# Optimization experiments

Measured on AMD Instinct MI355X. Metric: run time of the kernel, lower is better.

Reference implementation:

```python
import jax, jax.numpy as jnp
import numpy as np

S, B, D, H, O = 128, 16, 512, 512, 256  # seq_len, batch, input=hidden (required equal), hidden, output

def setup_inputs() -> dict:
    key = jax.random.key(0)
    ks = jax.random.split(key, 11)
    sD = 1.0 / np.sqrt(D)
    sH = 1.0 / np.sqrt(H)
    g = lambda k, shape, s: (jax.random.normal(k, shape, dtype=jnp.float32) * s)
    return {
        "x": g(ks[0], (S, B, D), 1.0),
        # LocalAttention (undefined in source; feature-wise softmax gating): Linear(H,H)
        "attn_w": g(ks[1], (D, H), sD), "attn_b": g(ks[2], (H,), sD),
        "in_w": g(ks[3], (D, H), sD), "in_b": g(ks[4], (H,), sD),      # the_in
        "ins_w": g(ks[5], (H, H), sH), "ins_b": g(ks[6], (H,), sH),    # inside
        "sus_w": g(ks[7], (H, H), sH), "sus_b": g(ks[8], (H,), sH),    # suspend_state
        "out_w": g(ks[9], (H, O), sH), "out_b": g(ks[10], (O,), sH),   # output_layer
    }

def reference(x, attn_w, attn_b, in_w, in_b, ins_w, ins_b, sus_w, sus_b, out_w, out_b):
    S_, B_, _ = x.shape
    H_ = ins_w.shape[0]

    def step(carry, read):
        watch, sus = carry  # both [S,B,H] per the original broadcasting bug/behavior
        a = jax.nn.softmax(read @ attn_w + attn_b, axis=-1)  # [B,H]
        r = a * read                                          # [B,D]
        # [B,H] broadcasts over leading S dim of [S,B,H]
        watch = jnp.tanh((r @ in_w + in_b) + (watch @ ins_w + ins_b))
        sus = jnp.tanh((watch @ sus_w + sus_b) + sus)
        out = watch @ out_w + out_b                           # [S,B,O]
        return (watch, sus), out

    init = (jnp.zeros((S_, B_, H_), x.dtype), jnp.zeros((S_, B_, H_), x.dtype))
    (watch, sus), outs = jax.lax.scan(step, init, x)  # outs: [S,S,B,O]
    return outs, watch, sus
```

## Files before the change

### kernel.cpp

```cpp
#include <hip/hip_runtime.h>
#include <hip/hip_bf16.h>
#include <math.h>


#define S_LEN 128
#define B_SZ  16
#define H_SZ  512
#define O_SZ  256
#define ROWS  (S_LEN * B_SZ)

#define OUTS_ELEMS  (S_LEN * S_LEN * B_SZ * O_SZ)
#define WATCH_ELEMS (S_LEN * B_SZ * H_SZ)

typedef float  f32x4  __attribute__((ext_vector_type(4)));
typedef __bf16 bf16x8 __attribute__((ext_vector_type(8)));

struct alignas(16) GemmLds {
  __bf16 Ah[64][40]; __bf16 Al[64][40];
  __bf16 Bh[64][40]; __bf16 Bl[64][40];
};

__device__ __forceinline__ void gemm_body(
    const float* __restrict__ A, const float* __restrict__ B,
    const float* __restrict__ bias0, const float* __restrict__ bias1,
    float* __restrict__ C, int N, int K, int bm, int bn, GemmLds& T)
{
  const int tid = threadIdx.x;
  const int w = tid >> 6, l = tid & 63;
  const int fr = l & 15, fg = l >> 4;
  f32x4 acc[4] = {{0,0,0,0},{0,0,0,0},{0,0,0,0},{0,0,0,0}};
  const int ar = tid >> 2, ak = (tid & 3) << 3;
  const int bk = tid >> 3, bc = (tid & 7) << 3;

  for (int k0 = 0; k0 < K; k0 += 32) {
    {
      const float* s = &A[(size_t)(bm + ar) * K + k0 + ak];
      const f32x4 v0 = *(const f32x4*)s, v1 = *(const f32x4*)(s + 4);
      const float vv[8] = {v0.x, v0.y, v0.z, v0.w, v1.x, v1.y, v1.z, v1.w};
      bf16x8 h, lo;
#pragma unroll
      for (int j = 0; j < 8; ++j) {
        const __bf16 hh = (__bf16)vv[j];
        h[j] = hh; lo[j] = (__bf16)(vv[j] - (float)hh);
      }
      *(bf16x8*)&T.Ah[ar][ak] = h;
      *(bf16x8*)&T.Al[ar][ak] = lo;
    }
    {
      const float* s = &B[(size_t)(k0 + bk) * N + bn + bc];
      const f32x4 v0 = *(const f32x4*)s, v1 = *(const f32x4*)(s + 4);
      const float vv[8] = {v0.x, v0.y, v0.z, v0.w, v1.x, v1.y, v1.z, v1.w};
#pragma unroll
      for (int j = 0; j < 8; ++j) {
        const __bf16 hh = (__bf16)vv[j];
        T.Bh[bc + j][bk] = hh;
        T.Bl[bc + j][bk] = (__bf16)(vv[j] - (float)hh);
      }
    }
    __syncthreads();
    const bf16x8 ah = *(const bf16x8*)&T.Ah[(w << 4) + fr][fg << 3];
    const bf16x8 al = *(const bf16x8*)&T.Al[(w << 4) + fr][fg << 3];
#pragma unroll
    for (int nr = 0; nr < 4; ++nr) {
      const bf16x8 bh = *(const bf16x8*)&T.Bh[(nr << 4) + fr][fg << 3];
      const bf16x8 bl = *(const bf16x8*)&T.Bl[(nr << 4) + fr][fg << 3];
      acc[nr] = __builtin_amdgcn_mfma_f32_16x16x32_bf16(ah, bh, acc[nr], 0, 0, 0);
      acc[nr] = __builtin_amdgcn_mfma_f32_16x16x32_bf16(al, bh, acc[nr], 0, 0, 0);
      acc[nr] = __builtin_amdgcn_mfma_f32_16x16x32_bf16(ah, bl, acc[nr], 0, 0, 0);
    }
    __syncthreads();
  }
#pragma unroll
  for (int nr = 0; nr < 4; ++nr) {
    const int gcol = bn + (nr << 4) + fr;
    float bb = bias0 ? bias0[gcol] : 0.f;
    if (bias1) bb += bias1[gcol];
#pragma unroll
    for (int r = 0; r < 4; ++r) {
      const int grow = bm + (w << 4) + (fg << 2) + r;
      C[(size_t)grow * N + gcol] = acc[nr][r] + bb;
    }
  }
}

__global__ __launch_bounds__(256) void gemm_mfma(
    const float* __restrict__ A, const float* __restrict__ B,
    const float* __restrict__ bias0, const float* __restrict__ bias1,
    float* __restrict__ C, int N, int K)
{
  __shared__ GemmLds T;
  gemm_body(A, B, bias0, bias1, C, N, K, blockIdx.y << 6, blockIdx.x << 6, T);
}

__global__ __launch_bounds__(256) void gemm_dual_mfma(
    const float* __restrict__ A,
    const float* __restrict__ B1, const float* __restrict__ b1, float* __restrict__ C1,
    const float* __restrict__ B2, const float* __restrict__ b2, float* __restrict__ C2)
{
  __shared__ GemmLds T;
  if (blockIdx.x < 8)
    gemm_body(A, B1, b1, nullptr, C1, 512, 512, blockIdx.y << 6, blockIdx.x << 6, T);
  else
    gemm_body(A, B2, b2, nullptr, C2, 256, 512, blockIdx.y << 6, (blockIdx.x - 8) << 6, T);
}

__global__ __launch_bounds__(64) void softmax_gate(float* __restrict__ lg,
                                                   const float* __restrict__ x)
{
  const int r = blockIdx.x;
  const int lane = threadIdx.x;
  float v[8];
  float m = -1e30f;
#pragma unroll
  for (int i = 0; i < 8; ++i) {
    v[i] = lg[(r << 9) + (i << 6) + lane];
    m = fmaxf(m, v[i]);
  }
#pragma unroll
  for (int off = 32; off > 0; off >>= 1) m = fmaxf(m, __shfl_xor(m, off, 64));
  float s = 0.f;
#pragma unroll
  for (int i = 0; i < 8; ++i) { v[i] = expf(v[i] - m); s += v[i]; }
#pragma unroll
  for (int off = 32; off > 0; off >>= 1) s += __shfl_xor(s, off, 64);
  const float inv = 1.0f / s;
#pragma unroll
  for (int i = 0; i < 8; ++i) {
    const int idx = (r << 9) + (i << 6) + lane;
    lg[idx] = v[i] * inv * x[idx];
  }
}

__global__ __launch_bounds__(256, 1) void recurrence(
    const float* __restrict__ cbuf,
    const float* __restrict__ insw,
    float* __restrict__ wall,
    unsigned long long* __restrict__ pz)
{
  __shared__ float wsm[H_SZ];
  __shared__ float red[2][4][64];

  const int wg  = blockIdx.x;
  const int b   = wg & 15;
  const int p   = wg >> 4;
  const int tid = threadIdx.x;
  const int cl  = tid & 63;
  const int kq  = tid >> 6;
  const int c   = (p << 6) + cl;
  const int kbase = kq << 7;

  f32x4 wr[32];
#pragma unroll
  for (int j = 0; j < 32; ++j) {
    wr[j].x = insw[((kbase + 4 * j + 0) << 9) + c];
    wr[j].y = insw[((kbase + 4 * j + 1) << 9) + c];
    wr[j].z = insw[((kbase + 4 * j + 2) << 9) + c];
    wr[j].w = insw[((kbase + 4 * j + 3) << 9) + c];
  }

  if (tid < 64) {
    const float v = tanhf(cbuf[(b << 9) + c]);
    wall[(b << 9) + c] = v;
    const unsigned long long pk =
        (1ULL << 32) | (unsigned long long)__float_as_uint(v);
    __hip_atomic_store(&pz[(b << 9) + c], pk, __ATOMIC_RELAXED,
                       __HIP_MEMORY_SCOPE_AGENT);
  }

  for (int t = 1; t < S_LEN; ++t) {
    const float cv = cbuf[(t << 13) + (b << 9) + c];

    const unsigned long long* src =
        pz + (((t - 1) & 15) << 13) + (b << 9);
    unsigned long long v0, v1;
    for (;;) {
      v0 = __hip_atomic_load(&src[2 * tid], __ATOMIC_RELAXED,
                             __HIP_MEMORY_SCOPE_AGENT);
      v1 = __hip_atomic_load(&src[2 * tid + 1], __ATOMIC_RELAXED,
                             __HIP_MEMORY_SCOPE_AGENT);
      const bool ok = ((unsigned)(v0 >> 32) == (unsigned)t) &
                      ((unsigned)(v1 >> 32) == (unsigned)t);
      if (__ballot(ok) == ~0ULL) break;
    }
    wsm[2 * tid]     = __uint_as_float((unsigned)v0);
    wsm[2 * tid + 1] = __uint_as_float((unsigned)v1);
    asm volatile("s_waitcnt lgkmcnt(0)" ::: "memory");
    __builtin_amdgcn_sched_barrier(0);

    float a0 = 0.f, a1 = 0.f, a2 = 0.f, a3 = 0.f;
#pragma unroll
    for (int j = 0; j < 32; ++j) {
      const f32x4 wv = *(const f32x4*)&wsm[kbase + (j << 2)];
      a0 = fmaf(wr[j].x, wv.x, a0);
      a1 = fmaf(wr[j].y, wv.y, a1);
      a2 = fmaf(wr[j].z, wv.z, a2);
      a3 = fmaf(wr[j].w, wv.w, a3);
    }
    red[t & 1][kq][cl] = (a0 + a1) + (a2 + a3);
    __syncthreads();
    if (tid < 64) {
      const float y = red[t & 1][0][cl] + red[t & 1][1][cl] +
                      red[t & 1][2][cl] + red[t & 1][3][cl];
      const float v = tanhf(cv + y);
      wall[(t << 13) + (b << 9) + c] = v;
      const unsigned long long pk =
          ((unsigned long long)(unsigned)(t + 1) << 32) |
          (unsigned long long)__float_as_uint(v);
      __hip_atomic_store(&pz[((t & 15) << 13) + (b << 9) + c], pk,
                         __ATOMIC_RELAXED, __HIP_MEMORY_SCOPE_AGENT);
    }
  }
}

__global__ __launch_bounds__(256) void sus_scan(
    const float* __restrict__ M, float* __restrict__ s_small)
{
  const int gid = blockIdx.x * blockDim.x + threadIdx.x;
  float s = 0.f;
  float n0 = M[gid];
  float n1 = M[(1 << 13) + gid];
  float n2 = M[(2 << 13) + gid];
  float n3 = M[(3 << 13) + gid];
  for (int t = 0; t < S_LEN - 4; ++t) {
    const float cur = n0;
    n0 = n1; n1 = n2; n2 = n3;
    n3 = M[((t + 4) << 13) + gid];
    s = tanhf(cur + s);
  }
  s = tanhf(n0 + s); s = tanhf(n1 + s); s = tanhf(n2 + s); s = tanhf(n3 + s);
  s_small[gid] = s;
}

__global__ __launch_bounds__(256) void finalize(
    const f32x4* __restrict__ os4, f32x4* __restrict__ outs4,
    const f32x4* __restrict__ w127, const f32x4* __restrict__ s4,
    f32x4* __restrict__ watch_out, f32x4* __restrict__ sus_out)
{
  const int gid = blockIdx.x * blockDim.x + threadIdx.x;
  const int stride = gridDim.x * blockDim.x;
  for (int i = gid; i < (1 << 24); i += stride) {
    const int o4 = i & 63;
    const int b  = (i >> 6) & 15;
    const int t  = i >> 17;
    __builtin_nontemporal_store(os4[(((t << 4) + b) << 6) + o4], &outs4[i]);
  }
  if (gid < (1 << 18)) {
    const int src = gid & 2047;
    __builtin_nontemporal_store(w127[src], &watch_out[gid]);
    __builtin_nontemporal_store(s4[src], &sus_out[gid]);
  }
}

extern "C" void kernel_launch(void* const* d_in, const int* in_sizes, int n_in,
                              void* d_out, int out_size, void* d_ws, size_t ws_size,
                              hipStream_t stream)
{
  const float* x      = (const float*)d_in[0];
  const float* attn_w = (const float*)d_in[1];
  const float* attn_b = (const float*)d_in[2];
  const float* in_w   = (const float*)d_in[3];
  const float* in_b   = (const float*)d_in[4];
  const float* ins_w  = (const float*)d_in[5];
  const float* ins_b  = (const float*)d_in[6];
  const float* sus_w  = (const float*)d_in[7];
  const float* sus_b  = (const float*)d_in[8];
  const float* out_w  = (const float*)d_in[9];
  const float* out_b  = (const float*)d_in[10];

  float* ws    = (float*)d_ws;
  float* cbuf  = ws;
  float* wallb = ws + (1 << 20);
  float* tmp   = ws + (2 << 20);
  float* mbuf  = tmp;
  unsigned long long* pz = (unsigned long long*)(ws + (3 << 20));
  float* obuf    = ws;
  float* s_small = ws + (1 << 19);

  float* outp   = (float*)d_out;
  float* watchp = outp + OUTS_ELEMS;
  float* susp   = watchp + WATCH_ELEMS;

  const dim3 blk(256);
  gemm_mfma<<<dim3(8, 32), blk, 0, stream>>>(x, attn_w, attn_b, nullptr, tmp, 512, 512);
  softmax_gate<<<dim3(2048), dim3(64), 0, stream>>>(tmp, x);
  gemm_mfma<<<dim3(8, 32), blk, 0, stream>>>(tmp, in_w, in_b, ins_b, cbuf, 512, 512);
  recurrence<<<dim3(128), blk, 0, stream>>>(cbuf, ins_w, wallb, pz);
  gemm_dual_mfma<<<dim3(12, 32), blk, 0, stream>>>(wallb, sus_w, sus_b, mbuf,
                                                   out_w, out_b, obuf);
  sus_scan<<<dim3(32), blk, 0, stream>>>(mbuf, s_small);
  finalize<<<dim3(4096), blk, 0, stream>>>(
      (const f32x4*)obuf, (f32x4*)d_out,
      (const f32x4*)(wallb + (127 << 13)), (const f32x4*)s_small,
      (f32x4*)watchp, (f32x4*)susp);
}
```

Baseline: 336.6 us.

## Fuse sus scan into finalize and reload recurrence weights from memory each step

The separate sus_scan kernel is dropped. Its work now runs in 8 extra blocks of the finalize kernel, which scan four columns per thread with vector loads and write the broadcast sus output directly. This removes one launch and the intermediate s_small buffer. The recurrence kernel also stops keeping its ins_w slice in 128 registers across the whole loop and instead reloads the 128 weights from global/L2 inside every timestep before the spin-wait, trading register pressure for repeated memory traffic on the serial critical path.

```diff
diff --git a/kernel.cpp b/kernel.cpp
--- a/kernel.cpp
+++ b/kernel.cpp
@@ -149,15 +149,6 @@
   const int c   = (p << 6) + cl;
   const int kbase = kq << 7;
 
-  f32x4 wr[32];
-#pragma unroll
-  for (int j = 0; j < 32; ++j) {
-    wr[j].x = insw[((kbase + 4 * j + 0) << 9) + c];
-    wr[j].y = insw[((kbase + 4 * j + 1) << 9) + c];
-    wr[j].z = insw[((kbase + 4 * j + 2) << 9) + c];
-    wr[j].w = insw[((kbase + 4 * j + 3) << 9) + c];
-  }
-
   if (tid < 64) {
     const float v = tanhf(cbuf[(b << 9) + c]);
     wall[(b << 9) + c] = v;
@@ -169,6 +160,11 @@
 
   for (int t = 1; t < S_LEN; ++t) {
     const float cv = cbuf[(t << 13) + (b << 9) + c];
+    float wrf[128];
+#pragma unroll
+    for (int j = 0; j < 128; ++j)
+      wrf[j] = insw[((kbase + j) << 9) + c];
+    __builtin_amdgcn_sched_barrier(0);
 
     const unsigned long long* src =
         pz + (((t - 1) & 15) << 13) + (b << 9);
@@ -191,10 +187,10 @@
 #pragma unroll
     for (int j = 0; j < 32; ++j) {
       const f32x4 wv = *(const f32x4*)&wsm[kbase + (j << 2)];
-      a0 = fmaf(wr[j].x, wv.x, a0);
-      a1 = fmaf(wr[j].y, wv.y, a1);
-      a2 = fmaf(wr[j].z, wv.z, a2);
-      a3 = fmaf(wr[j].w, wv.w, a3);
+      a0 = fmaf(wrf[4 * j + 0], wv.x, a0);
+      a1 = fmaf(wrf[4 * j + 1], wv.y, a1);
+      a2 = fmaf(wrf[4 * j + 2], wv.z, a2);
+      a3 = fmaf(wrf[4 * j + 3], wv.w, a3);
     }
     red[t & 1][kq][cl] = (a0 + a1) + (a2 + a3);
     __syncthreads();
@@ -212,42 +208,48 @@
   }
 }
 
-__global__ __launch_bounds__(256) void sus_scan(
-    const float* __restrict__ M, float* __restrict__ s_small)
-{
-  const int gid = blockIdx.x * blockDim.x + threadIdx.x;
-  float s = 0.f;
-  float n0 = M[gid];
-  float n1 = M[(1 << 13) + gid];
-  float n2 = M[(2 << 13) + gid];
-  float n3 = M[(3 << 13) + gid];
-  for (int t = 0; t < S_LEN - 4; ++t) {
-    const float cur = n0;
-    n0 = n1; n1 = n2; n2 = n3;
-    n3 = M[((t + 4) << 13) + gid];
-    s = tanhf(cur + s);
-  }
-  s = tanhf(n0 + s); s = tanhf(n1 + s); s = tanhf(n2 + s); s = tanhf(n3 + s);
-  s_small[gid] = s;
-}
-
 __global__ __launch_bounds__(256) void finalize(
     const f32x4* __restrict__ os4, f32x4* __restrict__ outs4,
-    const f32x4* __restrict__ w127, const f32x4* __restrict__ s4,
+    const f32x4* __restrict__ w127, const f32x4* __restrict__ M4,
     f32x4* __restrict__ watch_out, f32x4* __restrict__ sus_out)
 {
-  const int gid = blockIdx.x * blockDim.x + threadIdx.x;
-  const int stride = gridDim.x * blockDim.x;
-  for (int i = gid; i < (1 << 24); i += stride) {
-    const int o4 = i & 63;
-    const int b  = (i >> 6) & 15;
-    const int t  = i >> 17;
-    __builtin_nontemporal_store(os4[(((t << 4) + b) << 6) + o4], &outs4[i]);
-  }
-  if (gid < (1 << 18)) {
-    const int src = gid & 2047;
-    __builtin_nontemporal_store(w127[src], &watch_out[gid]);
-    __builtin_nontemporal_store(s4[src], &sus_out[gid]);
+  const int bid = blockIdx.x;
+  if (bid < 4096) {
+    const int gid = bid * 256 + threadIdx.x;
+    for (int i = gid; i < (1 << 24); i += 4096 * 256) {
+      const int o4 = i & 63;
+      const int b  = (i >> 6) & 15;
+      const int t  = i >> 17;
+      __builtin_nontemporal_store(os4[(((t << 4) + b) << 6) + o4], &outs4[i]);
+    }
+    if (gid < (1 << 18))
+      __builtin_nontemporal_store(w127[gid & 2047], &watch_out[gid]);
+  } else {
+    const int gid = (bid - 4096) * 256 + threadIdx.x;
+    f32x4 n0 = M4[gid];
+    f32x4 n1 = M4[(1 << 11) + gid];
+    f32x4 n2 = M4[(2 << 11) + gid];
+    f32x4 n3 = M4[(3 << 11) + gid];
+    float sx = 0.f, sy = 0.f, sz = 0.f, sw = 0.f;
+    for (int t = 0; t < S_LEN - 4; ++t) {
+      const f32x4 cur = n0;
+      n0 = n1; n1 = n2; n2 = n3;
+      n3 = M4[((t + 4) << 11) + gid];
+      sx = tanhf(cur.x + sx); sy = tanhf(cur.y + sy);
+      sz = tanhf(cur.z + sz); sw = tanhf(cur.w + sw);
+    }
+    sx = tanhf(n0.x + sx); sy = tanhf(n0.y + sy);
+    sz = tanhf(n0.z + sz); sw = tanhf(n0.w + sw);
+    sx = tanhf(n1.x + sx); sy = tanhf(n1.y + sy);
+    sz = tanhf(n1.z + sz); sw = tanhf(n1.w + sw);
+    sx = tanhf(n2.x + sx); sy = tanhf(n2.y + sy);
+    sz = tanhf(n2.z + sz); sw = tanhf(n2.w + sw);
+    sx = tanhf(n3.x + sx); sy = tanhf(n3.y + sy);
+    sz = tanhf(n3.z + sz); sw = tanhf(n3.w + sw);
+    const f32x4 s = {sx, sy, sz, sw};
+#pragma unroll 4
+    for (int si = 0; si < S_LEN; ++si)
+      __builtin_nontemporal_store(s, &sus_out[(si << 11) + gid]);
   }
 }
 
@@ -273,8 +275,7 @@
   float* tmp   = ws + (2 << 20);
   float* mbuf  = tmp;
   unsigned long long* pz = (unsigned long long*)(ws + (3 << 20));
-  float* obuf    = ws;
-  float* s_small = ws + (1 << 19);
+  float* obuf  = ws;
 
   float* outp   = (float*)d_out;
   float* watchp = outp + OUTS_ELEMS;
@@ -287,9 +288,8 @@
   recurrence<<<dim3(128), blk, 0, stream>>>(cbuf, ins_w, wallb, pz);
   gemm_dual_mfma<<<dim3(12, 32), blk, 0, stream>>>(wallb, sus_w, sus_b, mbuf,
                                                    out_w, out_b, obuf);
-  sus_scan<<<dim3(32), blk, 0, stream>>>(mbuf, s_small);
-  finalize<<<dim3(4096), blk, 0, stream>>>(
+  finalize<<<dim3(4104), blk, 0, stream>>>(
       (const f32x4*)obuf, (f32x4*)d_out,
-      (const f32x4*)(wallb + (127 << 13)), (const f32x4*)s_small,
+      (const f32x4*)(wallb + (127 << 13)), (const f32x4*)mbuf,
       (f32x4*)watchp, (f32x4*)susp);
 }
```

New measurement: 368.4 us. +9.4%, slower.
